# Kernel optimization log

Hardware: AMD Instinct MI355X
Metric: run time of the kernel (lower is better)

The kernel has to match this reference:

```python
import jax, jax.numpy as jnp
import numpy as np

BN_EPS = 1e-5

def _batchnorm(x):
    # BatchNorm1d(affine=False) in training mode: per-feature batch stats, biased var
    mu = jnp.mean(x, axis=0, keepdims=True)
    var = jnp.mean((x - mu) ** 2, axis=0, keepdims=True)
    return (x - mu) / jnp.sqrt(var + BN_EPS)

def setup_inputs() -> dict:
    key = jax.random.key(0)
    ks = jax.random.split(key, 8)
    H, I, S, E = 1024, 4096, 128, 16384  # hidden, intermediate, sqrt(experts), experts
    std = 0.02
    return {
        "hidden_states": jax.random.normal(ks[0], (4, 2048, H), jnp.float32),
        "gate_proj_weight": jax.random.normal(ks[1], (I, H), jnp.float32) * std,
        "up_proj_weight": jax.random.normal(ks[2], (I, H), jnp.float32) * std,
        "down_proj_weight": jax.random.normal(ks[3], (H, I), jnp.float32) * std,
        "router_gate_x_weight": jax.random.normal(ks[4], (S, H), jnp.float32) * std,
        "router_gate_y_weight": jax.random.normal(ks[5], (S, H), jnp.float32) * std,
        "up_embed": jax.random.normal(ks[6], (E, H), jnp.float32) * std,
        "down_embed": jax.random.normal(ks[7], (E, H), jnp.float32) * std,
        "top_k": 16,
    }

def reference(hidden_states, gate_proj_weight, up_proj_weight, down_proj_weight,
              router_gate_x_weight, router_gate_y_weight, up_embed, down_embed, top_k):
    bsz, seq_len, H = hidden_states.shape
    x = hidden_states.reshape(-1, H)  # [T, H]
    S = router_gate_x_weight.shape[0]  # num_expert_sqrt

    # dual-axis router: two small gates -> batchnorm -> log-softmax
    lpx = jax.nn.log_softmax(_batchnorm(x @ router_gate_x_weight.T), axis=-1)  # [T, S]
    lpy = jax.nn.log_softmax(_batchnorm(x @ router_gate_y_weight.T), axis=-1)  # [T, S]
    # combined log-prob over S*S experts: expert (i,j) -> i*S + j
    combined = (lpx[:, :, None] + lpy[:, None, :]).reshape(-1, S * S)  # [T, S*S]
    scores, indices = jax.lax.top_k(combined, top_k)  # [T, K]
    routing_weights = jnp.exp(scores)  # [T, K] = p_x * p_y

    # embedding-based expert: gather up/down rows, dot-scale-combine
    ue = up_embed[indices]    # [T, K, H]
    de = down_embed[indices]  # [T, K, H]
    up_score = jnp.einsum('tkh,th->tk', ue, x)          # per-expert scalar
    experts_states = jnp.einsum('tk,tkh->th', routing_weights * up_score, de)

    # dense SwiGLU MLP branch
    mlp = (jax.nn.silu(x @ gate_proj_weight.T) * (x @ up_proj_weight.T)) @ down_proj_weight.T

    out = mlp + experts_states
    return out.reshape(bsz, seq_len, H)
```

## Files before the change

kernel.cpp:

```cpp
#include <hip/hip_runtime.h>
#include <hip/hip_bf16.h>
#include <math.h>

#define T_TOK 8192
#define HDIM  1024
#define IDIM  4096
#define SDIM  128
#define TOPK  16

typedef __bf16 bf16x8 __attribute__((ext_vector_type(8)));
typedef float  f32x4  __attribute__((ext_vector_type(4)));

__device__ __forceinline__ unsigned short f2bf(float f) {
    union { float f; unsigned u; } a; a.f = f;
    unsigned r = a.u + 0x7fffu + ((a.u >> 16) & 1u);
    return (unsigned short)(r >> 16);
}
__device__ __forceinline__ float bf2f(unsigned short b) {
    union { unsigned u; float f; } a; a.u = ((unsigned)b) << 16;
    return a.f;
}

__device__ __forceinline__ void gld_lds16(const void* g, void* l) {
    __builtin_amdgcn_global_load_lds(
        (__attribute__((address_space(1))) void*)g,
        (__attribute__((address_space(3))) void*)l,
        16, 0, 0);
}

struct CvtSegs {
    const float4* src[8];
    ushort4*      dst[8];
    int           end[8];
};

__global__ __launch_bounds__(256)
void cvt_all_kernel(CvtSegs segs) {
    int i = blockIdx.x * 256 + threadIdx.x;
    if (i >= segs.end[7]) return;
    int s = 0;
    #pragma unroll
    for (int k = 0; k < 7; ++k) s += (i >= segs.end[k]) ? 1 : 0;
    int base = (s == 0) ? 0 : segs.end[s - 1];
    int j = i - base;
    float4 v = segs.src[s][j];
    ushort4 o;
    o.x = f2bf(v.x); o.y = f2bf(v.y); o.z = f2bf(v.z); o.w = f2bf(v.w);
    segs.dst[s][j] = o;
}

template<int ADD>
__global__ __launch_bounds__(256)
void gemm_bt(const unsigned short* __restrict__ A, const unsigned short* __restrict__ B,
             float* __restrict__ C, int M, int N, int K) {
    __shared__ unsigned short As[4096];
    __shared__ unsigned short Bs[4096];
    const int tid  = threadIdx.x;
    const int lane = tid & 63;
    const int wave = tid >> 6;
    const int tm = blockIdx.x * 128;
    const int tn = blockIdx.y * 128;
    const int wm = (wave & 1) * 64;
    const int wn = (wave >> 1) * 64;
    const int quad = lane >> 4;
    const int tr   = lane & 15;

    f32x4 acc[4][4] = {};
    bf16x8 af[4], bfr[4];

    const int ua0 = tid,        am0 = ua0 & 127, ak0 = ua0 >> 7;
    const int ua1 = tid + 256,  am1 = ua1 & 127, ak1 = ua1 >> 7;

    auto issue = [&](int kt) {
        gld_lds16(A + (size_t)(tm + am0) * K + kt + ak0 * 8, &As[ua0 * 8]);
        gld_lds16(A + (size_t)(tm + am1) * K + kt + ak1 * 8, &As[ua1 * 8]);
        gld_lds16(B + (size_t)(tn + am0) * K + kt + ak0 * 8, &Bs[ua0 * 8]);
        gld_lds16(B + (size_t)(tn + am1) * K + kt + ak1 * 8, &Bs[ua1 * 8]);
    };
    auto rdfrags = [&]() {
        #pragma unroll
        for (int mi = 0; mi < 4; ++mi)
            af[mi] = *(const bf16x8*)&As[(quad * 128 + wm + mi * 16 + tr) * 8];
        #pragma unroll
        for (int ni = 0; ni < 4; ++ni)
            bfr[ni] = *(const bf16x8*)&Bs[(quad * 128 + wn + ni * 16 + tr) * 8];
    };
    auto mfmas = [&]() {
        #pragma unroll
        for (int mi = 0; mi < 4; ++mi)
            #pragma unroll
            for (int ni = 0; ni < 4; ++ni)
                acc[mi][ni] = __builtin_amdgcn_mfma_f32_16x16x32_bf16(af[mi], bfr[ni], acc[mi][ni], 0, 0, 0);
    };

    issue(0);
    asm volatile("s_waitcnt vmcnt(0)" ::: "memory");
    __syncthreads();
    rdfrags();
    for (int kt = 32; kt < K; kt += 32) {
        __syncthreads();
        issue(kt);
        mfmas();
        asm volatile("s_waitcnt vmcnt(0)" ::: "memory");
        __syncthreads();
        rdfrags();
    }
    mfmas();

    #pragma unroll
    for (int mi = 0; mi < 4; ++mi) {
        #pragma unroll
        for (int ni = 0; ni < 4; ++ni) {
            int col = tn + wn + ni * 16 + tr;
            #pragma unroll
            for (int r = 0; r < 4; ++r) {
                int row = tm + wm + mi * 16 + quad * 4 + r;
                size_t o = (size_t)row * N + col;
                float v = acc[mi][ni][r];
                if (ADD) v += C[o];
                C[o] = v;
            }
        }
    }
}

#define BARX() asm volatile("s_barrier" ::: "memory")
#define VMW(n) asm volatile("s_waitcnt vmcnt(" #n ")" ::: "memory")

#define RD_A(r, MB) { const char* _p = lds + ((r) << 14); \
    af[0] = *(const bf16x8*)(_p + aoff[(MB)+0]); \
    af[1] = *(const bf16x8*)(_p + aoff[(MB)+1]); \
    af[2] = *(const bf16x8*)(_p + aoff[(MB)+2]); \
    af[3] = *(const bf16x8*)(_p + aoff[(MB)+3]); }

#define RD_B(r) { const char* _p = lds + 65536 + ((r) << 14); \
    bfv[0] = *(const bf16x8*)(_p + boff[0]); \
    bfv[1] = *(const bf16x8*)(_p + boff[1]); \
    bfv[2] = *(const bf16x8*)(_p + boff[2]); \
    bfv[3] = *(const bf16x8*)(_p + boff[3]); }

#define MMA16(ACC) { __builtin_amdgcn_s_setprio(1); \
    _Pragma("unroll") \
    for (int _i = 0; _i < 4; ++_i) \
        _Pragma("unroll") \
        for (int _n = 0; _n < 4; ++_n) \
            ACC[_i][_n] = __builtin_amdgcn_mfma_f32_16x16x32_bf16(af[_i], bfv[_n], ACC[_i][_n], 0, 0, 0); \
    __builtin_amdgcn_s_setprio(0); }

__global__ __launch_bounds__(512, 2)
void gemm1_8ph(const unsigned short* __restrict__ Xb, const unsigned short* __restrict__ Wg,
               const unsigned short* __restrict__ Wu, unsigned short* __restrict__ Hb) {
    __shared__ __align__(16) char lds[131072];
    const int tid  = threadIdx.x;
    const int lane = tid & 63;
    const int wid  = tid >> 6;
    const int quad = lane >> 4;
    const int tr   = lane & 15;
    const int wm   = (wid >> 2) << 7;
    const int wn   = (wid & 3) << 6;

    const int bid = blockIdx.x;
    const int u   = bid >> 3;
    const int gm  = (((bid & 7) << 2) | (u & 3)) << 8;
    const int gn  = (u >> 2) << 8;

    const int vsw  = (tid & 7) ^ ((tid >> 3) & 7);
    const int rowb = ((tid >> 3) << 1) | (vsw >> 2);
    const int cq8  = (vsw & 3) << 3;

    const unsigned short* pA0 = Xb + (size_t)(gm + rowb) * HDIM + cq8;
    const unsigned short* pA1 = pA0 + (size_t)128 * HDIM;
    auto wsrc = [&](int R) -> const unsigned short* {
        const unsigned short* base = ((R >> 4) & 1) ? Wu : Wg;
        int sr = ((R >> 5) << 4) | (R & 15);
        return base + (size_t)sr * HDIM + cq8;
    };
    const unsigned short* pB0 = wsrc(gn + rowb);
    const unsigned short* pB1 = wsrc(gn + rowb + 128);

    int aoff[8], boff[4];
    #pragma unroll
    for (int i = 0; i < 8; ++i) {
        int row = wm + i * 16 + tr;
        aoff[i] = ((row >> 1) << 7) | (((((row & 1) << 2) | quad) ^ ((row >> 1) & 7)) << 4);
    }
    #pragma unroll
    for (int i = 0; i < 4; ++i) {
        int row = wn + i * 16 + tr;
        boff[i] = ((row >> 1) << 7) | (((((row & 1) << 2) | quad) ^ ((row >> 1) & 7)) << 4);
    }

    f32x4 accL[4][4] = {};
    f32x4 accH[4][4] = {};
    bf16x8 af[4], bfv[4];

    auto stageA = [&](int slot, int kOff) {
        char* d = lds + (slot << 14) + (tid << 4);
        gld_lds16(pA0 + kOff, d);
        gld_lds16(pA1 + kOff, d + 8192);
    };
    auto stageB = [&](int slot, int kOff) {
        char* d = lds + 65536 + (slot << 14) + (tid << 4);
        gld_lds16(pB0 + kOff, d);
        gld_lds16(pB1 + kOff, d + 8192);
    };

    stageA(0, 0);  stageB(0, 0);
    stageA(1, 32); stageB(1, 32);
    stageA(2, 64); stageB(2, 64);
    VMW(8); BARX();

    for (int t = 0; t < 32; ++t) {
        const int r  = t & 3;
        const int rn = (t + 3) & 3;
        const int kN = (t < 29 ? t + 3 : 31) << 5;
        RD_A(r, 0); RD_B(r);
        stageA(rn, kN);
        MMA16(accL);
        RD_A(r, 4);
        stageB(rn, kN);
        MMA16(accH);
        VMW(8); BARX();
    }
    asm volatile("s_waitcnt vmcnt(0)" ::: "memory");

    const size_t icb = (size_t)((gn + wn) >> 1) + tr;
    const int rbase = gm + wm + quad * 4;
    #pragma unroll
    for (int mi = 0; mi < 4; ++mi) {
        #pragma unroll
        for (int p = 0; p < 2; ++p) {
            #pragma unroll
            for (int r = 0; r < 4; ++r) {
                {
                    float g = accL[mi][2 * p][r], u2 = accL[mi][2 * p + 1][r];
                    float h = g / (1.0f + __expf(-g)) * u2;
                    Hb[(size_t)(rbase + mi * 16 + r) * IDIM + icb + 16 * p] = f2bf(h);
                }
                {
                    float g = accH[mi][2 * p][r], u2 = accH[mi][2 * p + 1][r];
                    float h = g / (1.0f + __expf(-g)) * u2;
                    Hb[(size_t)(rbase + 64 + mi * 16 + r) * IDIM + icb + 16 * p] = f2bf(h);
                }
            }
        }
    }
}

#define RD2_A(r) { const char* _p = lds + ((r) << 14); \
    _Pragma("unroll") \
    for (int _i = 0; _i < 8; ++_i) af[_i] = *(const bf16x8*)(_p + aoff[_i]); }

#define RD2_B(r) { const char* _p = lds + 65536 + ((r) << 13); \
    bfv[0] = *(const bf16x8*)(_p + boff[0]); \
    bfv[1] = *(const bf16x8*)(_p + boff[1]); }

#define MMA2() { __builtin_amdgcn_s_setprio(1); \
    _Pragma("unroll") \
    for (int _i = 0; _i < 8; ++_i) \
        _Pragma("unroll") \
        for (int _n = 0; _n < 2; ++_n) \
            acc[_i][_n] = __builtin_amdgcn_mfma_f32_16x16x32_bf16(af[_i], bfv[_n], acc[_i][_n], 0, 0, 0); \
    __builtin_amdgcn_s_setprio(0); }

__global__ __launch_bounds__(512, 2)
void gemm2_8ph(const unsigned short* __restrict__ A, const unsigned short* __restrict__ B,
               float* __restrict__ C) {
    __shared__ __align__(16) char lds[98304];
    const int K = IDIM, N = HDIM;
    const int tid  = threadIdx.x;
    const int lane = tid & 63;
    const int wid  = tid >> 6;
    const int quad = lane >> 4;
    const int tr   = lane & 15;
    const int wm   = (wid >> 2) << 7;
    const int wn   = (wid & 3) << 5;

    const int bid = blockIdx.x;
    const int u   = bid >> 3;
    const int gm  = (((bid & 7) << 2) | (u >> 3)) << 8;
    const int gn  = (u & 7) << 7;

    const int vsw  = (tid & 7) ^ ((tid >> 3) & 7);
    const int rowb = ((tid >> 3) << 1) | (vsw >> 2);
    const int cq8  = (vsw & 3) << 3;

    const unsigned short* pA0 = A + (size_t)(gm + rowb) * K + cq8;
    const unsigned short* pA1 = pA0 + (size_t)128 * K;
    const unsigned short* pB0 = B + (size_t)(gn + rowb) * K + cq8;

    int aoff[8], boff[2];
    #pragma unroll
    for (int i = 0; i < 8; ++i) {
        int row = wm + i * 16 + tr;
        aoff[i] = ((row >> 1) << 7) | (((((row & 1) << 2) | quad) ^ ((row >> 1) & 7)) << 4);
    }
    #pragma unroll
    for (int i = 0; i < 2; ++i) {
        int row = wn + i * 16 + tr;
        boff[i] = ((row >> 1) << 7) | (((((row & 1) << 2) | quad) ^ ((row >> 1) & 7)) << 4);
    }

    f32x4 acc[8][2] = {};
    bf16x8 af[8], bfv[2];

    auto stageA = [&](int slot, int kOff) {
        char* d = lds + (slot << 14) + (tid << 4);
        gld_lds16(pA0 + kOff, d);
        gld_lds16(pA1 + kOff, d + 8192);
    };
    auto stageB = [&](int slot, int kOff) {
        char* d = lds + 65536 + (slot << 13) + (tid << 4);
        gld_lds16(pB0 + kOff, d);
    };

    stageA(0, 0);  stageB(0, 0);
    stageA(1, 32); stageB(1, 32);
    stageA(2, 64); stageB(2, 64);
    VMW(6); BARX();

    for (int t = 0; t < 128; ++t) {
        const int r  = t & 3;
        const int rn = (t + 3) & 3;
        const int kN = (t < 125 ? t + 3 : 127) << 5;
        RD2_A(r); RD2_B(r);
        stageA(rn, kN); stageB(rn, kN);
        MMA2();
        VMW(6); BARX();
    }
    asm volatile("s_waitcnt vmcnt(0)" ::: "memory");

    #pragma unroll
    for (int mi = 0; mi < 8; ++mi) {
        #pragma unroll
        for (int ni = 0; ni < 2; ++ni) {
            int col = gn + wn + ni * 16 + tr;
            #pragma unroll
            for (int r = 0; r < 4; ++r) {
                int row = gm + wm + mi * 16 + quad * 4 + r;
                size_t o = (size_t)row * N + col;
                C[o] += acc[mi][ni][r];
            }
        }
    }
}

__global__ void bn_stats(const float* __restrict__ gxy, float* __restrict__ sums, float* __restrict__ ssq) {
    const int j = threadIdx.x;
    const int b = blockIdx.x;
    float s = 0.f, q = 0.f;
    for (int r = 0; r < 32; ++r) {
        float v = gxy[(size_t)(b * 32 + r) * 256 + j];
        s += v; q += v * v;
    }
    atomicAdd(&sums[j], s);
    atomicAdd(&ssq[j], q);
}

__global__ __launch_bounds__(256)
void routing_kernel(const float* __restrict__ gxy, const float* __restrict__ sums,
                    const float* __restrict__ ssq, int* __restrict__ oidx, float* __restrict__ owt) {
    const int lane = threadIdx.x & 63;
    const int t = blockIdx.x * 4 + (threadIdx.x >> 6);
    const float invT = 1.0f / (float)T_TOK;
    const float* g = gxy + (size_t)t * 256;

    float z[4];
    const int cols[4] = {lane, lane + 64, 128 + lane, 192 + lane};
    #pragma unroll
    for (int i = 0; i < 4; ++i) {
        int c = cols[i];
        float mu  = sums[c] * invT;
        float var = ssq[c] * invT - mu * mu;
        z[i] = (g[c] - mu) * rsqrtf(var + 1e-5f);
    }
    float mx = fmaxf(z[0], z[1]);
    float my = fmaxf(z[2], z[3]);
    #pragma unroll
    for (int m = 32; m >= 1; m >>= 1) {
        mx = fmaxf(mx, __shfl_xor(mx, m));
        my = fmaxf(my, __shfl_xor(my, m));
    }
    float sx = __expf(z[0] - mx) + __expf(z[1] - mx);
    float sy = __expf(z[2] - my) + __expf(z[3] - my);
    #pragma unroll
    for (int m = 32; m >= 1; m >>= 1) {
        sx += __shfl_xor(sx, m);
        sy += __shfl_xor(sy, m);
    }
    float lx0 = z[0] - (mx + __logf(sx)), lx1 = z[1] - (mx + __logf(sx));
    float ly0 = z[2] - (my + __logf(sy)), ly1 = z[3] - (my + __logf(sy));

    float aw = -INFINITY; int ai = 0;
    float bw = -INFINITY; int bi = 0;
    {
        float v0 = lx0, v1 = lx1;
        for (int i = 0; i < 16; ++i) {
            float v; int c;
            if (v0 >= v1) { v = v0; c = lane; } else { v = v1; c = lane + 64; }
            #pragma unroll
            for (int m = 32; m >= 1; m >>= 1) {
                float ov = __shfl_xor(v, m); int oc = __shfl_xor(c, m);
                if (ov > v || (ov == v && oc < c)) { v = ov; c = oc; }
            }
            if ((c & 63) == lane) { if (c < 64) v0 = -INFINITY; else v1 = -INFINITY; }
            if (lane == i) { aw = v; ai = c; }
        }
    }
    {
        float v0 = ly0, v1 = ly1;
        for (int i = 0; i < 16; ++i) {
            float v; int c;
            if (v0 >= v1) { v = v0; c = lane; } else { v = v1; c = lane + 64; }
            #pragma unroll
            for (int m = 32; m >= 1; m >>= 1) {
                float ov = __shfl_xor(v, m); int oc = __shfl_xor(c, m);
                if (ov > v || (ov == v && oc < c)) { v = ov; c = oc; }
            }
            if ((c & 63) == lane) { if (c < 64) v0 = -INFINITY; else v1 = -INFINITY; }
            if (lane == i) { bw = v; bi = c; }
        }
    }
    float cv[4];
    #pragma unroll
    for (int j = 0; j < 4; ++j) {
        int c = lane + 64 * j;
        cv[j] = __shfl(aw, c >> 4) + __shfl(bw, c & 15);
    }
    int myidx = 0; float myw = 0.f;
    for (int i = 0; i < 16; ++i) {
        float v = cv[0]; int c = lane;
        #pragma unroll
        for (int j = 1; j < 4; ++j) { int cc = lane + 64 * j; if (cv[j] > v) { v = cv[j]; c = cc; } }
        #pragma unroll
        for (int m = 32; m >= 1; m >>= 1) {
            float ov = __shfl_xor(v, m); int oc = __shfl_xor(c, m);
            if (ov > v || (ov == v && oc < c)) { v = ov; c = oc; }
        }
        #pragma unroll
        for (int j = 0; j < 4; ++j) if (c == lane + 64 * j) cv[j] = -INFINITY;
        int p = c >> 4, q = c & 15;
        int ex = __shfl(ai, p);
        int ey = __shfl(bi, q);
        if (lane == i) { myidx = ex * 128 + ey; myw = __expf(v); }
    }
    if (lane < 16) {
        oidx[t * TOPK + lane] = myidx;
        owt[t * TOPK + lane]  = myw;
    }
}

__global__ __launch_bounds__(256)
void expert_combine(const unsigned short* __restrict__ xb, const int* __restrict__ idx,
                    const float* __restrict__ wts, const unsigned short* __restrict__ ueb,
                    const unsigned short* __restrict__ deb, float* __restrict__ out) {
    const int t = blockIdx.x;
    const int tid = threadIdx.x;
    const int lane = tid & 63, wv = tid >> 6;
    __shared__ float part[TOPK * 4];
    __shared__ float sc[TOPK];
    ushort4 xv4 = ((const ushort4*)(xb + (size_t)t * HDIM))[tid];
    float x0 = bf2f(xv4.x), x1 = bf2f(xv4.y), x2 = bf2f(xv4.z), x3 = bf2f(xv4.w);
    int e[TOPK];
    #pragma unroll
    for (int k = 0; k < TOPK; ++k) e[k] = idx[t * TOPK + k];
    #pragma unroll
    for (int k = 0; k < TOPK; ++k) {
        ushort4 u4 = ((const ushort4*)(ueb + (size_t)e[k] * HDIM))[tid];
        float p = bf2f(u4.x) * x0 + bf2f(u4.y) * x1 + bf2f(u4.z) * x2 + bf2f(u4.w) * x3;
        #pragma unroll
        for (int m = 32; m >= 1; m >>= 1) p += __shfl_xor(p, m);
        if (lane == 0) part[k * 4 + wv] = p;
    }
    __syncthreads();
    if (tid < TOPK) {
        float s = part[tid * 4] + part[tid * 4 + 1] + part[tid * 4 + 2] + part[tid * 4 + 3];
        sc[tid] = s * wts[t * TOPK + tid];
    }
    __syncthreads();
    float4 acc = {0.f, 0.f, 0.f, 0.f};
    #pragma unroll
    for (int k = 0; k < TOPK; ++k) {
        float s = sc[k];
        ushort4 d4 = ((const ushort4*)(deb + (size_t)e[k] * HDIM))[tid];
        acc.x += s * bf2f(d4.x); acc.y += s * bf2f(d4.y);
        acc.z += s * bf2f(d4.z); acc.w += s * bf2f(d4.w);
    }
    ((float4*)(out + (size_t)t * HDIM))[tid] = acc;
}

extern "C" void kernel_launch(void* const* d_in, const int* in_sizes, int n_in,
                              void* d_out, int out_size, void* d_ws, size_t ws_size,
                              hipStream_t stream) {
    const float* x  = (const float*)d_in[0];
    const float* gw = (const float*)d_in[1];
    const float* uw = (const float*)d_in[2];
    const float* dw = (const float*)d_in[3];
    const float* wx = (const float*)d_in[4];
    const float* wy = (const float*)d_in[5];
    const float* ue = (const float*)d_in[6];
    const float* de = (const float*)d_in[7];
    float* out = (float*)d_out;

    char* ws = (char*)d_ws;
    size_t o = 0;
    auto alloc = [&](size_t bytes) { void* p = ws + o; o += (bytes + 255) & ~(size_t)255; return p; };
    unsigned short* xb    = (unsigned short*)alloc((size_t)T_TOK * HDIM * 2);
    unsigned short* gateb = (unsigned short*)alloc((size_t)IDIM * HDIM * 2);
    unsigned short* upb   = (unsigned short*)alloc((size_t)IDIM * HDIM * 2);
    unsigned short* downb = (unsigned short*)alloc((size_t)HDIM * IDIM * 2);
    unsigned short* wrb   = (unsigned short*)alloc((size_t)256 * HDIM * 2);
    unsigned short* ueb   = (unsigned short*)alloc((size_t)16384 * HDIM * 2);
    unsigned short* deb   = (unsigned short*)alloc((size_t)16384 * HDIM * 2);
    unsigned short* hbuf  = (unsigned short*)alloc((size_t)T_TOK * IDIM * 2);
    float* gxy  = (float*)alloc((size_t)T_TOK * 256 * 4);
    float* sums = (float*)alloc(256 * 4);
    float* ssq  = (float*)alloc(256 * 4);
    int*   idxs = (int*)alloc((size_t)T_TOK * TOPK * 4);
    float* wts  = (float*)alloc((size_t)T_TOK * TOPK * 4);

    CvtSegs segs;
    const float* srcs[8] = {x, gw, uw, dw, wx, wy, ue, de};
    unsigned short* dsts[8] = {xb, gateb, upb, downb, wrb, wrb + SDIM * HDIM, ueb, deb};
    const int cnt4[8] = {T_TOK * HDIM / 4, IDIM * HDIM / 4, IDIM * HDIM / 4, IDIM * HDIM / 4,
                         SDIM * HDIM / 4, SDIM * HDIM / 4, 16384 * HDIM / 4, 16384 * HDIM / 4};
    int acc = 0;
    for (int i = 0; i < 8; ++i) {
        segs.src[i] = (const float4*)srcs[i];
        segs.dst[i] = (ushort4*)dsts[i];
        acc += cnt4[i];
        segs.end[i] = acc;
    }
    cvt_all_kernel<<<(acc + 255) / 256, 256, 0, stream>>>(segs);

    hipMemsetAsync(sums, 0, 2 * 256 * 4, stream);
    gemm_bt<0><<<dim3(T_TOK / 128, 256 / 128), 256, 0, stream>>>(xb, wrb, gxy, T_TOK, 256, HDIM);
    bn_stats<<<256, 256, 0, stream>>>(gxy, sums, ssq);
    routing_kernel<<<T_TOK / 4, 256, 0, stream>>>(gxy, sums, ssq, idxs, wts);

    expert_combine<<<T_TOK, 256, 0, stream>>>(xb, idxs, wts, ueb, deb, out);

    gemm1_8ph<<<1024, 512, 0, stream>>>(xb, gateb, upb, hbuf);
    gemm2_8ph<<<256, 512, 0, stream>>>(hbuf, downb, out);
}
```

Measured before the change: 641.9 us.

## Double-buffer LDS fragments in both GEMMs and reshape gemm2 wave tiles

Both MFMA GEMM kernels now load the next k-step's A/B fragments from LDS into a second register set while the current set feeds the MFMAs. Scheduling barriers keep the LDS reads and MFMAs from being interleaved by the compiler, and the A and B global-to-LDS copies are merged into one staging call with adjusted vmcnt waits. The down-projection GEMM also changes each wave's tile from 128x32 to 64x64, so each MFMA needs fewer LDS fragment reads. The cost is roughly double the fragment registers, which may pressure occupancy at 2 blocks of 512 threads.

```diff
diff --git a/kernel.cpp b/kernel.cpp
--- a/kernel.cpp
+++ b/kernel.cpp
@@ -127,24 +127,24 @@
 #define BARX() asm volatile("s_barrier" ::: "memory")
 #define VMW(n) asm volatile("s_waitcnt vmcnt(" #n ")" ::: "memory")
 
-#define RD_A(r, MB) { const char* _p = lds + ((r) << 14); \
-    af[0] = *(const bf16x8*)(_p + aoff[(MB)+0]); \
-    af[1] = *(const bf16x8*)(_p + aoff[(MB)+1]); \
-    af[2] = *(const bf16x8*)(_p + aoff[(MB)+2]); \
-    af[3] = *(const bf16x8*)(_p + aoff[(MB)+3]); }
-
-#define RD_B(r) { const char* _p = lds + 65536 + ((r) << 14); \
-    bfv[0] = *(const bf16x8*)(_p + boff[0]); \
-    bfv[1] = *(const bf16x8*)(_p + boff[1]); \
-    bfv[2] = *(const bf16x8*)(_p + boff[2]); \
-    bfv[3] = *(const bf16x8*)(_p + boff[3]); }
-
-#define MMA16(ACC) { __builtin_amdgcn_s_setprio(1); \
+#define RDT1(AF, BV, r) { const char* _pa = lds + ((r) << 14); \
+    const char* _pb = lds + 65536 + ((r) << 14); \
+    _Pragma("unroll") \
+    for (int _i = 0; _i < 8; ++_i) AF[_i] = *(const bf16x8*)(_pa + aoff[_i]); \
+    _Pragma("unroll") \
+    for (int _n = 0; _n < 4; ++_n) BV[_n] = *(const bf16x8*)(_pb + boff[_n]); }
+
+#define MMAT1(AF, BV) { __builtin_amdgcn_s_setprio(1); \
     _Pragma("unroll") \
     for (int _i = 0; _i < 4; ++_i) \
         _Pragma("unroll") \
         for (int _n = 0; _n < 4; ++_n) \
-            ACC[_i][_n] = __builtin_amdgcn_mfma_f32_16x16x32_bf16(af[_i], bfv[_n], ACC[_i][_n], 0, 0, 0); \
+            accL[_i][_n] = __builtin_amdgcn_mfma_f32_16x16x32_bf16(AF[_i], BV[_n], accL[_i][_n], 0, 0, 0); \
+    _Pragma("unroll") \
+    for (int _i = 0; _i < 4; ++_i) \
+        _Pragma("unroll") \
+        for (int _n = 0; _n < 4; ++_n) \
+            accH[_i][_n] = __builtin_amdgcn_mfma_f32_16x16x32_bf16(AF[_i + 4], BV[_n], accH[_i][_n], 0, 0, 0); \
     __builtin_amdgcn_s_setprio(0); }
 
 __global__ __launch_bounds__(512, 2)
@@ -192,35 +192,35 @@
 
     f32x4 accL[4][4] = {};
     f32x4 accH[4][4] = {};
-    bf16x8 af[4], bfv[4];
-
-    auto stageA = [&](int slot, int kOff) {
-        char* d = lds + (slot << 14) + (tid << 4);
-        gld_lds16(pA0 + kOff, d);
-        gld_lds16(pA1 + kOff, d + 8192);
+    bf16x8 afA[8], bvA[4], afB[8], bvB[4];
+
+    auto stageAB = [&](int slot, int kOff) {
+        char* da = lds + (slot << 14) + (tid << 4);
+        char* db = lds + 65536 + (slot << 14) + (tid << 4);
+        gld_lds16(pA0 + kOff, da);
+        gld_lds16(pA1 + kOff, da + 8192);
+        gld_lds16(pB0 + kOff, db);
+        gld_lds16(pB1 + kOff, db + 8192);
     };
-    auto stageB = [&](int slot, int kOff) {
-        char* d = lds + 65536 + (slot << 14) + (tid << 4);
-        gld_lds16(pB0 + kOff, d);
-        gld_lds16(pB1 + kOff, d + 8192);
-    };
-
-    stageA(0, 0);  stageB(0, 0);
-    stageA(1, 32); stageB(1, 32);
-    stageA(2, 64); stageB(2, 64);
-    VMW(8); BARX();
-
-    for (int t = 0; t < 32; ++t) {
-        const int r  = t & 3;
-        const int rn = (t + 3) & 3;
-        const int kN = (t < 29 ? t + 3 : 31) << 5;
-        RD_A(r, 0); RD_B(r);
-        stageA(rn, kN);
-        MMA16(accL);
-        RD_A(r, 4);
-        stageB(rn, kN);
-        MMA16(accH);
-        VMW(8); BARX();
+
+    stageAB(0, 0);
+    stageAB(1, 32);
+    stageAB(2, 64);
+    VMW(4); BARX();
+    RDT1(afA, bvA, 0);
+
+    for (int tt = 0; tt < 16; ++tt) {
+        const int t0 = tt * 2, t1 = t0 + 1;
+        RDT1(afB, bvB, t1 & 3);
+        { int ts = t0 + 3; stageAB(ts & 3, (ts <= 31 ? ts : 31) << 5); }
+        __builtin_amdgcn_sched_barrier(0);
+        MMAT1(afA, bvA);
+        VMW(4); BARX();
+        RDT1(afA, bvA, (t1 + 1) & 3);
+        { int ts = t1 + 3; stageAB(ts & 3, (ts <= 31 ? ts : 31) << 5); }
+        __builtin_amdgcn_sched_barrier(0);
+        MMAT1(afB, bvB);
+        VMW(4); BARX();
     }
     asm volatile("s_waitcnt vmcnt(0)" ::: "memory");
 
@@ -247,20 +247,19 @@
     }
 }
 
-#define RD2_A(r) { const char* _p = lds + ((r) << 14); \
-    _Pragma("unroll") \
-    for (int _i = 0; _i < 8; ++_i) af[_i] = *(const bf16x8*)(_p + aoff[_i]); }
-
-#define RD2_B(r) { const char* _p = lds + 65536 + ((r) << 13); \
-    bfv[0] = *(const bf16x8*)(_p + boff[0]); \
-    bfv[1] = *(const bf16x8*)(_p + boff[1]); }
-
-#define MMA2() { __builtin_amdgcn_s_setprio(1); \
-    _Pragma("unroll") \
-    for (int _i = 0; _i < 8; ++_i) \
+#define RDT2(AF, BV, r) { const char* _pa = lds + ((r) << 14); \
+    const char* _pb = lds + 65536 + ((r) << 13); \
+    _Pragma("unroll") \
+    for (int _i = 0; _i < 4; ++_i) AF[_i] = *(const bf16x8*)(_pa + aoff[_i]); \
+    _Pragma("unroll") \
+    for (int _n = 0; _n < 4; ++_n) BV[_n] = *(const bf16x8*)(_pb + boff[_n]); }
+
+#define MMAT2(AF, BV) { __builtin_amdgcn_s_setprio(1); \
+    _Pragma("unroll") \
+    for (int _i = 0; _i < 4; ++_i) \
         _Pragma("unroll") \
-        for (int _n = 0; _n < 2; ++_n) \
-            acc[_i][_n] = __builtin_amdgcn_mfma_f32_16x16x32_bf16(af[_i], bfv[_n], acc[_i][_n], 0, 0, 0); \
+        for (int _n = 0; _n < 4; ++_n) \
+            acc[_i][_n] = __builtin_amdgcn_mfma_f32_16x16x32_bf16(AF[_i], BV[_n], acc[_i][_n], 0, 0, 0); \
     __builtin_amdgcn_s_setprio(0); }
 
 __global__ __launch_bounds__(512, 2)
@@ -273,8 +272,8 @@
     const int wid  = tid >> 6;
     const int quad = lane >> 4;
     const int tr   = lane & 15;
-    const int wm   = (wid >> 2) << 7;
-    const int wn   = (wid & 3) << 5;
+    const int wm   = (wid >> 1) << 6;
+    const int wn   = (wid & 1) << 6;
 
     const int bid = blockIdx.x;
     const int u   = bid >> 3;
@@ -289,51 +288,54 @@
     const unsigned short* pA1 = pA0 + (size_t)128 * K;
     const unsigned short* pB0 = B + (size_t)(gn + rowb) * K + cq8;
 
-    int aoff[8], boff[2];
-    #pragma unroll
-    for (int i = 0; i < 8; ++i) {
+    int aoff[4], boff[4];
+    #pragma unroll
+    for (int i = 0; i < 4; ++i) {
         int row = wm + i * 16 + tr;
         aoff[i] = ((row >> 1) << 7) | (((((row & 1) << 2) | quad) ^ ((row >> 1) & 7)) << 4);
     }
     #pragma unroll
-    for (int i = 0; i < 2; ++i) {
+    for (int i = 0; i < 4; ++i) {
         int row = wn + i * 16 + tr;
         boff[i] = ((row >> 1) << 7) | (((((row & 1) << 2) | quad) ^ ((row >> 1) & 7)) << 4);
     }
 
-    f32x4 acc[8][2] = {};
-    bf16x8 af[8], bfv[2];
-
-    auto stageA = [&](int slot, int kOff) {
-        char* d = lds + (slot << 14) + (tid << 4);
-        gld_lds16(pA0 + kOff, d);
-        gld_lds16(pA1 + kOff, d + 8192);
+    f32x4 acc[4][4] = {};
+    bf16x8 afA[4], bvA[4], afB[4], bvB[4];
+
+    auto stageAB = [&](int slot, int kOff) {
+        char* da = lds + (slot << 14) + (tid << 4);
+        char* db = lds + 65536 + (slot << 13) + (tid << 4);
+        gld_lds16(pA0 + kOff, da);
+        gld_lds16(pA1 + kOff, da + 8192);
+        gld_lds16(pB0 + kOff, db);
     };
-    auto stageB = [&](int slot, int kOff) {
-        char* d = lds + 65536 + (slot << 13) + (tid << 4);
-        gld_lds16(pB0 + kOff, d);
-    };
-
-    stageA(0, 0);  stageB(0, 0);
-    stageA(1, 32); stageB(1, 32);
-    stageA(2, 64); stageB(2, 64);
-    VMW(6); BARX();
-
-    for (int t = 0; t < 128; ++t) {
-        const int r  = t & 3;
-        const int rn = (t + 3) & 3;
-        const int kN = (t < 125 ? t + 3 : 127) << 5;
-        RD2_A(r); RD2_B(r);
-        stageA(rn, kN); stageB(rn, kN);
-        MMA2();
-        VMW(6); BARX();
+
+    stageAB(0, 0);
+    stageAB(1, 32);
+    stageAB(2, 64);
+    VMW(3); BARX();
+    RDT2(afA, bvA, 0);
+
+    for (int tt = 0; tt < 64; ++tt) {
+        const int t0 = tt * 2, t1 = t0 + 1;
+        RDT2(afB, bvB, t1 & 3);
+        { int ts = t0 + 3; stageAB(ts & 3, (ts <= 127 ? ts : 127) << 5); }
+        __builtin_amdgcn_sched_barrier(0);
+        MMAT2(afA, bvA);
+        VMW(3); BARX();
+        RDT2(afA, bvA, (t1 + 1) & 3);
+        { int ts = t1 + 3; stageAB(ts & 3, (ts <= 127 ? ts : 127) << 5); }
+        __builtin_amdgcn_sched_barrier(0);
+        MMAT2(afB, bvB);
+        VMW(3); BARX();
     }
     asm volatile("s_waitcnt vmcnt(0)" ::: "memory");
 
     #pragma unroll
-    for (int mi = 0; mi < 8; ++mi) {
-        #pragma unroll
-        for (int ni = 0; ni < 2; ++ni) {
+    for (int mi = 0; mi < 4; ++mi) {
+        #pragma unroll
+        for (int ni = 0; ni < 4; ++ni) {
             int col = gn + wn + ni * 16 + tr;
             #pragma unroll
             for (int r = 0; r < 4; ++r) {
```

Result: no change. 641.6 us (-0.0%).
